# Kernel tuning notes

Measured on AMD Instinct MI355X. Metric: run time of the kernel, lower is better.

## Reference

```python
import jax, jax.numpy as jnp
import numpy as np

N_NODES = 100000
N_EDGES = 1000000
N_GRAPHS = 16
CUTOFF = 6.0
ETAS = [0.5, 1.0, 2.0, 4.0]
OFFSETS = [0.0, 1.0, 2.0, 3.0, 4.0, 5.0, 6.0, 7.0]
SPECIES = (0, 1, 2)


def setup_inputs() -> dict:
    key = jax.random.key(0)
    ks = jax.random.split(key, 6)
    pos = jax.random.normal(ks[0], (N_NODES, 3), dtype=jnp.float32)
    cell = jax.random.normal(ks[1], (N_GRAPHS, 3, 3), dtype=jnp.float32)
    edge_shift = jax.random.normal(ks[2], (N_EDGES, 3), dtype=jnp.float32)
    z = jax.random.randint(ks[3], (N_NODES,), 0, 3, dtype=jnp.int64)
    edge_index = jax.random.randint(ks[4], (2, N_EDGES), 0, N_NODES, dtype=jnp.int64)
    batch = jnp.sort(jax.random.randint(ks[5], (N_NODES,), 0, N_GRAPHS, dtype=jnp.int64))
    # buffers from torch.cartesian_prod(etas, offsets).t(): etas repeated, offsets tiled
    etas = jnp.repeat(jnp.asarray(ETAS, dtype=jnp.float32), len(OFFSETS))      # [P]
    offsets = jnp.tile(jnp.asarray(OFFSETS, dtype=jnp.float32), len(ETAS))     # [P]
    return {"pos": pos, "cell": cell, "edge_shift": edge_shift, "etas": etas,
            "offsets": offsets, "z": z, "edge_index": edge_index, "batch": batch}


def reference(pos, cell, edge_shift, etas, offsets, z, edge_index, batch):
    i = edge_index[0]  # receiver
    j = edge_index[1]  # sender
    # periodic-image-shifted edge vectors: [E,3]
    vec_ij = pos[j] - pos[i] + jnp.einsum('ni,nij->nj', edge_shift, cell[batch[i]])
    r_ij = jnp.linalg.norm(vec_ij, axis=-1)  # [E]
    # cosine cutoff
    fc = jnp.where(r_ij < CUTOFF, 0.5 * (jnp.cos(jnp.pi * r_ij / CUTOFF) + 1.0), 0.0)
    # Gaussian RBF per (eta, offset) pair: [P, E]
    G2_ij = jnp.exp(-etas[:, None] * (r_ij - offsets[:, None]) ** 2 / CUTOFF ** 2) * fc
    zj = z[j]
    outs = []
    for sp in SPECIES:  # small fixed loop over species (3)
        m = (zj == sp).astype(G2_ij.dtype)          # [E]
        seg = jax.ops.segment_sum((G2_ij * m).T, i, num_segments=pos.shape[0])  # [N, P]
        outs.append(seg.T)                           # [P, N]
    return jnp.concatenate(outs, axis=0)             # [S*P, N]
```

## Files before the change

### kernel.cpp

```cpp
#include <hip/hip_runtime.h>
#include <math.h>

#define N_NODES 100000
#define N_EDGES 1000000
#define NPAIR 32
#define CUTOFF 6.0f

#define CHUNK 512
#define NCHUNK 196
#define HALF 256

#define NT_BIN 256
#define EPT 10
#define EPB (NT_BIN * EPT)
#define NB_BIN ((N_EDGES + EPB - 1) / EPB)

#define SLICE 32
#define PAYLOAD 31
#define NODECAP 32
#define BSTRIDE 33

#define NB_ACC (NCHUNK * 2)


__global__ __launch_bounds__(256) void pack_kernel(
    const float* __restrict__ pos,
    const int*   __restrict__ z,
    const int*   __restrict__ batch,
    float4*      __restrict__ packed)
{
    int n = blockIdx.x * 256 + threadIdx.x;
    if (n < N_NODES) {
        float4 p;
        p.x = pos[3 * n + 0];
        p.y = pos[3 * n + 1];
        p.z = pos[3 * n + 2];
        p.w = __int_as_float((z[n] & 3) | (batch[n] << 2));
        packed[n] = p;
    }
}

__global__ __launch_bounds__(NT_BIN, 1) void bin_kernel(
    const float4* __restrict__ packed,
    const float*  __restrict__ cell,
    const float*  __restrict__ shift,
    const int*    __restrict__ ei,
    unsigned int* __restrict__ bucket)
{
    __shared__ int lhist[NCHUNK];
    int tid = threadIdx.x;
    int blk = blockIdx.x;

    if (tid < NCHUNK) lhist[tid] = 0;
    __syncthreads();

    int base = blk * EPB;

    int iv[EPT], jv[EPT];
    float sx[EPT], sy[EPT], sz[EPT];
    bool val[EPT];
#pragma unroll
    for (int q = 0; q < EPT; ++q) {
        int e = base + tid + q * NT_BIN;
        val[q] = (e < N_EDGES);
        int ee = val[q] ? e : 0;
        iv[q] = ei[ee];
        jv[q] = ei[N_EDGES + ee];
        sx[q] = shift[3 * ee + 0];
        sy[q] = shift[3 * ee + 1];
        sz[q] = shift[3 * ee + 2];
    }

    float4 fi[EPT], fj[EPT];
#pragma unroll
    for (int q = 0; q < EPT; ++q) {
        fi[q] = packed[iv[q]];
        fj[q] = packed[jv[q]];
    }

#pragma unroll
    for (int q = 0; q < EPT; ++q) {
        if (val[q]) {
            int bi = __float_as_int(fi[q].w) >> 2;
            int zj = __float_as_int(fj[q].w) & 3;
            const float* C = cell + 9 * bi;
            float vx = fj[q].x - fi[q].x + sx[q] * C[0] + sy[q] * C[3] + sz[q] * C[6];
            float vy = fj[q].y - fi[q].y + sx[q] * C[1] + sy[q] * C[4] + sz[q] * C[7];
            float vz = fj[q].z - fi[q].z + sx[q] * C[2] + sy[q] * C[5] + sz[q] * C[8];
            float r = sqrtf(vx * vx + vy * vy + vz * vz);
            if (r < CUTOFF) {
                unsigned int qq = (unsigned int)(r * (2097152.0f / 6.0f));
                qq = min(qq, 2097151u);
                int c = iv[q] >> 9;
                unsigned int rec = (qq << 11) | ((unsigned int)(iv[q] & 511) << 2)
                                 | (unsigned int)zj;
                int loc = atomicAdd(&lhist[c], 1);
                if (loc < PAYLOAD)
                    bucket[((size_t)c * NB_BIN + blk) * SLICE + loc] = rec;
            }
        }
    }
    __syncthreads();

    if (tid < NCHUNK) {
        unsigned int h = (unsigned int)min(lhist[tid], PAYLOAD);
        bucket[((size_t)tid * NB_BIN + blk) * SLICE + PAYLOAD] = h;
    }
}

__global__ __launch_bounds__(256, 1) void accum_kernel(
    const unsigned int* __restrict__ bucket,
    float*              __restrict__ out)
{
    __shared__ unsigned int bins[HALF * BSTRIDE];
    __shared__ int lcur[HALF];
    __shared__ int scnt[NB_BIN];
    int tid = threadIdx.x;
    int chunk = blockIdx.x >> 1;
    int half  = blockIdx.x & 1;
    int locbase = half * HALF;

    lcur[tid] = 0;
    for (int s = tid; s < NB_BIN; s += 256)
        scnt[s] = (int)bucket[((size_t)chunk * NB_BIN + s) * SLICE + PAYLOAD];
    __syncthreads();

    const uint4* b4 = (const uint4*)(bucket + (size_t)chunk * NB_BIN * SLICE);
    const int n4 = NB_BIN * (SLICE / 4);

    for (int k = tid; k < n4; k += 256) {
        uint4 v = b4[k];
        int s  = k >> 3;
        int w0 = (k & 7) << 2;
        int cnt = scnt[s];
        unsigned int rr[4] = {v.x, v.y, v.z, v.w};
#pragma unroll
        for (int u = 0; u < 4; ++u) {
            if (w0 + u < cnt) {
                unsigned int rc = rr[u];
                int l = (int)((rc >> 2) & 511) - locbase;
                if ((unsigned)l < HALF) {
                    int slot = atomicAdd(&lcur[l], 1);
                    if (slot < NODECAP) bins[l * BSTRIDE + slot] = rc;
                }
            }
        }
    }
    __syncthreads();

    int n = min(lcur[tid], NODECAP);
    float a0[NPAIR], a1[NPAIR], a2[NPAIR];
#pragma unroll
    for (int p = 0; p < NPAIR; ++p) { a0[p] = 0.0f; a1[p] = 0.0f; a2[p] = 0.0f; }

    for (int k = 0; k < n; ++k) {
        unsigned int rc = bins[tid * BSTRIDE + k];
        int spec = rc & 3;
        float r = (float)(rc >> 11) * (6.0f / 2097152.0f);
        float fc = 0.5f * (__cosf(r * (float)(M_PI / 6.0)) + 1.0f);
        float m0 = (spec == 0) ? fc : 0.0f;
        float m1 = (spec == 1) ? fc : 0.0f;
        float m2 = (spec == 2) ? fc : 0.0f;
#pragma unroll
        for (int o = 0; o < 8; ++o) {
            float d = r - (float)o;
            float e0 = __expf(d * d * (-0.5f / 36.0f));
            float e1 = e0 * e0;
            float e2 = e1 * e1;
            float e3 = e2 * e2;
            a0[o]      = fmaf(m0, e0, a0[o]);
            a1[o]      = fmaf(m1, e0, a1[o]);
            a2[o]      = fmaf(m2, e0, a2[o]);
            a0[8 + o]  = fmaf(m0, e1, a0[8 + o]);
            a1[8 + o]  = fmaf(m1, e1, a1[8 + o]);
            a2[8 + o]  = fmaf(m2, e1, a2[8 + o]);
            a0[16 + o] = fmaf(m0, e2, a0[16 + o]);
            a1[16 + o] = fmaf(m1, e2, a1[16 + o]);
            a2[16 + o] = fmaf(m2, e2, a2[16 + o]);
            a0[24 + o] = fmaf(m0, e3, a0[24 + o]);
            a1[24 + o] = fmaf(m1, e3, a1[24 + o]);
            a2[24 + o] = fmaf(m2, e3, a2[24 + o]);
        }
    }

    int node = chunk * CHUNK + locbase + tid;
    if (node < N_NODES) {
#pragma unroll
        for (int p = 0; p < NPAIR; ++p) {
            out[(size_t)(0 * NPAIR + p) * N_NODES + node] = a0[p];
            out[(size_t)(1 * NPAIR + p) * N_NODES + node] = a1[p];
            out[(size_t)(2 * NPAIR + p) * N_NODES + node] = a2[p];
        }
    }
}

extern "C" void kernel_launch(void* const* d_in, const int* in_sizes, int n_in,
                              void* d_out, int out_size, void* d_ws, size_t ws_size,
                              hipStream_t stream) {
    const float* pos   = (const float*)d_in[0];
    const float* cell  = (const float*)d_in[1];
    const float* shift = (const float*)d_in[2];
    const int*   z     = (const int*)d_in[5];
    const int*   ei    = (const int*)d_in[6];
    const int*   batch = (const int*)d_in[7];
    float* out = (float*)d_out;

    char* ws = (char*)d_ws;
    unsigned int* bucket = (unsigned int*)ws;
    float4*       packed = (float4*)(ws + 9809408);

    int pblocks = (N_NODES + 255) / 256;
    pack_kernel<<<pblocks, 256, 0, stream>>>(pos, z, batch, packed);
    bin_kernel<<<NB_BIN, NT_BIN, 0, stream>>>(packed, cell, shift, ei, bucket);
    accum_kernel<<<NB_ACC, 256, 0, stream>>>(bucket, out);
}
```

Baseline: 54.45 us.

## Fuse pack, bin and accumulate kernels into one persistent kernel with grid barriers

Merges the three launches into a single kernel of 392 blocks that runs packing, edge binning and per-node accumulation as phases separated by software grid barriers built on global atomic counters. This removes inter-kernel launch gaps and tail drain. It relies on all blocks being co-resident to avoid deadlock, and adds a memset for barrier counters plus spin-wait costs. The larger combined register footprint under the new launch bounds may also affect the accumulation phase.

```diff
diff --git a/kernel.cpp b/kernel.cpp
--- a/kernel.cpp
+++ b/kernel.cpp
@@ -6,190 +6,197 @@
 #define NPAIR 32
 #define CUTOFF 6.0f
 
+#define NB 392
+#define NT 256
+
 #define CHUNK 512
 #define NCHUNK 196
 #define HALF 256
 
-#define NT_BIN 256
 #define EPT 10
-#define EPB (NT_BIN * EPT)
-#define NB_BIN ((N_EDGES + EPB - 1) / EPB)
+#define EPB (NT * EPT)
 
 #define SLICE 32
 #define PAYLOAD 31
 #define NODECAP 32
 #define BSTRIDE 33
 
-#define NB_ACC (NCHUNK * 2)
-
-
-__global__ __launch_bounds__(256) void pack_kernel(
+
+__global__ __launch_bounds__(NT, 2) void fused_kernel(
     const float* __restrict__ pos,
+    const float* __restrict__ cell,
+    const float* __restrict__ shift,
     const int*   __restrict__ z,
+    const int*   __restrict__ ei,
     const int*   __restrict__ batch,
-    float4*      __restrict__ packed)
-{
-    int n = blockIdx.x * 256 + threadIdx.x;
-    if (n < N_NODES) {
-        float4 p;
-        p.x = pos[3 * n + 0];
-        p.y = pos[3 * n + 1];
-        p.z = pos[3 * n + 2];
-        p.w = __int_as_float((z[n] & 3) | (batch[n] << 2));
-        packed[n] = p;
-    }
-}
-
-__global__ __launch_bounds__(NT_BIN, 1) void bin_kernel(
-    const float4* __restrict__ packed,
-    const float*  __restrict__ cell,
-    const float*  __restrict__ shift,
-    const int*    __restrict__ ei,
-    unsigned int* __restrict__ bucket)
+    int*          __restrict__ barcnt,
+    float4*       __restrict__ packed,
+    unsigned int* __restrict__ bucket,
+    float*        __restrict__ out)
 {
     __shared__ int lhist[NCHUNK];
-    int tid = threadIdx.x;
-    int blk = blockIdx.x;
-
-    if (tid < NCHUNK) lhist[tid] = 0;
-    __syncthreads();
-
-    int base = blk * EPB;
-
-    int iv[EPT], jv[EPT];
-    float sx[EPT], sy[EPT], sz[EPT];
-    bool val[EPT];
-#pragma unroll
-    for (int q = 0; q < EPT; ++q) {
-        int e = base + tid + q * NT_BIN;
-        val[q] = (e < N_EDGES);
-        int ee = val[q] ? e : 0;
-        iv[q] = ei[ee];
-        jv[q] = ei[N_EDGES + ee];
-        sx[q] = shift[3 * ee + 0];
-        sy[q] = shift[3 * ee + 1];
-        sz[q] = shift[3 * ee + 2];
-    }
-
-    float4 fi[EPT], fj[EPT];
-#pragma unroll
-    for (int q = 0; q < EPT; ++q) {
-        fi[q] = packed[iv[q]];
-        fj[q] = packed[jv[q]];
-    }
-
-#pragma unroll
-    for (int q = 0; q < EPT; ++q) {
-        if (val[q]) {
-            int bi = __float_as_int(fi[q].w) >> 2;
-            int zj = __float_as_int(fj[q].w) & 3;
-            const float* C = cell + 9 * bi;
-            float vx = fj[q].x - fi[q].x + sx[q] * C[0] + sy[q] * C[3] + sz[q] * C[6];
-            float vy = fj[q].y - fi[q].y + sx[q] * C[1] + sy[q] * C[4] + sz[q] * C[7];
-            float vz = fj[q].z - fi[q].z + sx[q] * C[2] + sy[q] * C[5] + sz[q] * C[8];
-            float r = sqrtf(vx * vx + vy * vy + vz * vz);
-            if (r < CUTOFF) {
-                unsigned int qq = (unsigned int)(r * (2097152.0f / 6.0f));
-                qq = min(qq, 2097151u);
-                int c = iv[q] >> 9;
-                unsigned int rec = (qq << 11) | ((unsigned int)(iv[q] & 511) << 2)
-                                 | (unsigned int)zj;
-                int loc = atomicAdd(&lhist[c], 1);
-                if (loc < PAYLOAD)
-                    bucket[((size_t)c * NB_BIN + blk) * SLICE + loc] = rec;
-            }
-        }
-    }
-    __syncthreads();
-
-    if (tid < NCHUNK) {
-        unsigned int h = (unsigned int)min(lhist[tid], PAYLOAD);
-        bucket[((size_t)tid * NB_BIN + blk) * SLICE + PAYLOAD] = h;
-    }
-}
-
-__global__ __launch_bounds__(256, 1) void accum_kernel(
-    const unsigned int* __restrict__ bucket,
-    float*              __restrict__ out)
-{
     __shared__ unsigned int bins[HALF * BSTRIDE];
     __shared__ int lcur[HALF];
-    __shared__ int scnt[NB_BIN];
-    int tid = threadIdx.x;
-    int chunk = blockIdx.x >> 1;
-    int half  = blockIdx.x & 1;
-    int locbase = half * HALF;
-
-    lcur[tid] = 0;
-    for (int s = tid; s < NB_BIN; s += 256)
-        scnt[s] = (int)bucket[((size_t)chunk * NB_BIN + s) * SLICE + PAYLOAD];
-    __syncthreads();
-
-    const uint4* b4 = (const uint4*)(bucket + (size_t)chunk * NB_BIN * SLICE);
-    const int n4 = NB_BIN * (SLICE / 4);
-
-    for (int k = tid; k < n4; k += 256) {
-        uint4 v = b4[k];
-        int s  = k >> 3;
-        int w0 = (k & 7) << 2;
-        int cnt = scnt[s];
-        unsigned int rr[4] = {v.x, v.y, v.z, v.w};
-#pragma unroll
-        for (int u = 0; u < 4; ++u) {
-            if (w0 + u < cnt) {
-                unsigned int rc = rr[u];
-                int l = (int)((rc >> 2) & 511) - locbase;
-                if ((unsigned)l < HALF) {
-                    int slot = atomicAdd(&lcur[l], 1);
-                    if (slot < NODECAP) bins[l * BSTRIDE + slot] = rc;
+    __shared__ int scnt[NB];
+
+    const int tid = threadIdx.x;
+    const int blk = blockIdx.x;
+
+    int gt = blk * NT + tid;
+    if (gt < N_NODES) {
+        float4 p;
+        p.x = pos[3 * gt + 0];
+        p.y = pos[3 * gt + 1];
+        p.z = pos[3 * gt + 2];
+        p.w = __int_as_float((z[gt] & 3) | (batch[gt] << 2));
+        packed[gt] = p;
+    }
+    if (tid < NCHUNK) lhist[tid] = 0;
+
+    __syncthreads();
+    if (tid == 0) {
+        __threadfence();
+        atomicAdd(&barcnt[0], 1);
+        while (atomicAdd(&barcnt[0], 0) < NB) { }
+        __threadfence();
+    }
+    __syncthreads();
+
+    {
+        int base = blk * EPB;
+        int iv[EPT], jv[EPT];
+        float sx[EPT], sy[EPT], sz[EPT];
+        bool val[EPT];
+#pragma unroll
+        for (int q = 0; q < EPT; ++q) {
+            int e = base + tid + q * NT;
+            val[q] = (e < N_EDGES);
+            int ee = val[q] ? e : 0;
+            iv[q] = ei[ee];
+            jv[q] = ei[N_EDGES + ee];
+            sx[q] = shift[3 * ee + 0];
+            sy[q] = shift[3 * ee + 1];
+            sz[q] = shift[3 * ee + 2];
+        }
+        float4 fi[EPT], fj[EPT];
+#pragma unroll
+        for (int q = 0; q < EPT; ++q) {
+            fi[q] = packed[iv[q]];
+            fj[q] = packed[jv[q]];
+        }
+#pragma unroll
+        for (int q = 0; q < EPT; ++q) {
+            if (val[q]) {
+                int bi = __float_as_int(fi[q].w) >> 2;
+                int zj = __float_as_int(fj[q].w) & 3;
+                const float* C = cell + 9 * bi;
+                float vx = fj[q].x - fi[q].x + sx[q] * C[0] + sy[q] * C[3] + sz[q] * C[6];
+                float vy = fj[q].y - fi[q].y + sx[q] * C[1] + sy[q] * C[4] + sz[q] * C[7];
+                float vz = fj[q].z - fi[q].z + sx[q] * C[2] + sy[q] * C[5] + sz[q] * C[8];
+                float r = sqrtf(vx * vx + vy * vy + vz * vz);
+                if (r < CUTOFF) {
+                    unsigned int qq = (unsigned int)(r * (2097152.0f / 6.0f));
+                    qq = min(qq, 2097151u);
+                    int c = iv[q] >> 9;
+                    unsigned int rec = (qq << 11) | ((unsigned int)(iv[q] & 511) << 2)
+                                     | (unsigned int)zj;
+                    int loc = atomicAdd(&lhist[c], 1);
+                    if (loc < PAYLOAD)
+                        bucket[((size_t)c * NB + blk) * SLICE + loc] = rec;
                 }
             }
         }
-    }
-    __syncthreads();
-
-    int n = min(lcur[tid], NODECAP);
-    float a0[NPAIR], a1[NPAIR], a2[NPAIR];
-#pragma unroll
-    for (int p = 0; p < NPAIR; ++p) { a0[p] = 0.0f; a1[p] = 0.0f; a2[p] = 0.0f; }
-
-    for (int k = 0; k < n; ++k) {
-        unsigned int rc = bins[tid * BSTRIDE + k];
-        int spec = rc & 3;
-        float r = (float)(rc >> 11) * (6.0f / 2097152.0f);
-        float fc = 0.5f * (__cosf(r * (float)(M_PI / 6.0)) + 1.0f);
-        float m0 = (spec == 0) ? fc : 0.0f;
-        float m1 = (spec == 1) ? fc : 0.0f;
-        float m2 = (spec == 2) ? fc : 0.0f;
-#pragma unroll
-        for (int o = 0; o < 8; ++o) {
-            float d = r - (float)o;
-            float e0 = __expf(d * d * (-0.5f / 36.0f));
-            float e1 = e0 * e0;
-            float e2 = e1 * e1;
-            float e3 = e2 * e2;
-            a0[o]      = fmaf(m0, e0, a0[o]);
-            a1[o]      = fmaf(m1, e0, a1[o]);
-            a2[o]      = fmaf(m2, e0, a2[o]);
-            a0[8 + o]  = fmaf(m0, e1, a0[8 + o]);
-            a1[8 + o]  = fmaf(m1, e1, a1[8 + o]);
-            a2[8 + o]  = fmaf(m2, e1, a2[8 + o]);
-            a0[16 + o] = fmaf(m0, e2, a0[16 + o]);
-            a1[16 + o] = fmaf(m1, e2, a1[16 + o]);
-            a2[16 + o] = fmaf(m2, e2, a2[16 + o]);
-            a0[24 + o] = fmaf(m0, e3, a0[24 + o]);
-            a1[24 + o] = fmaf(m1, e3, a1[24 + o]);
-            a2[24 + o] = fmaf(m2, e3, a2[24 + o]);
-        }
-    }
-
-    int node = chunk * CHUNK + locbase + tid;
-    if (node < N_NODES) {
-#pragma unroll
-        for (int p = 0; p < NPAIR; ++p) {
-            out[(size_t)(0 * NPAIR + p) * N_NODES + node] = a0[p];
-            out[(size_t)(1 * NPAIR + p) * N_NODES + node] = a1[p];
-            out[(size_t)(2 * NPAIR + p) * N_NODES + node] = a2[p];
+        __syncthreads();
+        if (tid < NCHUNK) {
+            unsigned int h = (unsigned int)min(lhist[tid], PAYLOAD);
+            bucket[((size_t)tid * NB + blk) * SLICE + PAYLOAD] = h;
+        }
+    }
+
+    __syncthreads();
+    if (tid == 0) {
+        __threadfence();
+        atomicAdd(&barcnt[1], 1);
+        while (atomicAdd(&barcnt[1], 0) < NB) { }
+        __threadfence();
+    }
+    __syncthreads();
+
+    {
+        int chunk = blk >> 1;
+        int half  = blk & 1;
+        int locbase = half * HALF;
+
+        lcur[tid] = 0;
+        for (int s = tid; s < NB; s += NT)
+            scnt[s] = (int)bucket[((size_t)chunk * NB + s) * SLICE + PAYLOAD];
+        __syncthreads();
+
+        const uint4* b4 = (const uint4*)(bucket + (size_t)chunk * NB * SLICE);
+        const int n4 = NB * (SLICE / 4);
+        for (int k = tid; k < n4; k += NT) {
+            uint4 v = b4[k];
+            int s  = k >> 3;
+            int w0 = (k & 7) << 2;
+            int cnt = scnt[s];
+            unsigned int rr[4] = {v.x, v.y, v.z, v.w};
+#pragma unroll
+            for (int u = 0; u < 4; ++u) {
+                if (w0 + u < cnt) {
+                    unsigned int rc = rr[u];
+                    int l = (int)((rc >> 2) & 511) - locbase;
+                    if ((unsigned)l < HALF) {
+                        int slot = atomicAdd(&lcur[l], 1);
+                        if (slot < NODECAP) bins[l * BSTRIDE + slot] = rc;
+                    }
+                }
+            }
+        }
+        __syncthreads();
+
+        int n = min(lcur[tid], NODECAP);
+        float a0[NPAIR], a1[NPAIR], a2[NPAIR];
+#pragma unroll
+        for (int p = 0; p < NPAIR; ++p) { a0[p] = 0.0f; a1[p] = 0.0f; a2[p] = 0.0f; }
+
+        for (int k = 0; k < n; ++k) {
+            unsigned int rc = bins[tid * BSTRIDE + k];
+            int spec = rc & 3;
+            float r = (float)(rc >> 11) * (6.0f / 2097152.0f);
+            float fc = 0.5f * (__cosf(r * (float)(M_PI / 6.0)) + 1.0f);
+            float m0 = (spec == 0) ? fc : 0.0f;
+            float m1 = (spec == 1) ? fc : 0.0f;
+            float m2 = (spec == 2) ? fc : 0.0f;
+#pragma unroll
+            for (int o = 0; o < 8; ++o) {
+                float d = r - (float)o;
+                float e0 = __expf(d * d * (-0.5f / 36.0f));
+                float e1 = e0 * e0;
+                float e2 = e1 * e1;
+                float e3 = e2 * e2;
+                a0[o]      = fmaf(m0, e0, a0[o]);
+                a1[o]      = fmaf(m1, e0, a1[o]);
+                a2[o]      = fmaf(m2, e0, a2[o]);
+                a0[8 + o]  = fmaf(m0, e1, a0[8 + o]);
+                a1[8 + o]  = fmaf(m1, e1, a1[8 + o]);
+                a2[8 + o]  = fmaf(m2, e1, a2[8 + o]);
+                a0[16 + o] = fmaf(m0, e2, a0[16 + o]);
+                a1[16 + o] = fmaf(m1, e2, a1[16 + o]);
+                a2[16 + o] = fmaf(m2, e2, a2[16 + o]);
+                a0[24 + o] = fmaf(m0, e3, a0[24 + o]);
+                a1[24 + o] = fmaf(m1, e3, a1[24 + o]);
+                a2[24 + o] = fmaf(m2, e3, a2[24 + o]);
+            }
+        }
+
+        int node = chunk * CHUNK + locbase + tid;
+        if (node < N_NODES) {
+#pragma unroll
+            for (int p = 0; p < NPAIR; ++p) {
+                out[(size_t)(0 * NPAIR + p) * N_NODES + node] = a0[p];
+                out[(size_t)(1 * NPAIR + p) * N_NODES + node] = a1[p];
+                out[(size_t)(2 * NPAIR + p) * N_NODES + node] = a2[p];
+            }
         }
     }
 }
@@ -206,11 +213,11 @@
     float* out = (float*)d_out;
 
     char* ws = (char*)d_ws;
-    unsigned int* bucket = (unsigned int*)ws;
-    float4*       packed = (float4*)(ws + 9809408);
-
-    int pblocks = (N_NODES + 255) / 256;
-    pack_kernel<<<pblocks, 256, 0, stream>>>(pos, z, batch, packed);
-    bin_kernel<<<NB_BIN, NT_BIN, 0, stream>>>(packed, cell, shift, ei, bucket);
-    accum_kernel<<<NB_ACC, 256, 0, stream>>>(bucket, out);
+    int*          barcnt = (int*)ws;
+    unsigned int* bucket = (unsigned int*)(ws + 64);
+    float4*       packed = (float4*)(ws + 64 + 9834496);
+
+    hipMemsetAsync(barcnt, 0, 2 * sizeof(int), stream);
+    fused_kernel<<<NB, NT, 0, stream>>>(pos, cell, shift, z, ei, batch,
+                                        barcnt, packed, bucket, out);
 }
```

Measured after the change: 144.1 us. 2.65x slower.
